# Kernel tuning notes

Hardware: AMD Instinct MI355X
Metric: run time of the kernel (lower is better)

The kernel has to match this reference:

```python
import jax, jax.numpy as jnp
import numpy as np

H = 16          # num_attention_heads
DH = 64         # attention_head_size = hidden // heads
WINDOW = 128    # window_size
GLOBAL_RATIO = 0.1
SCALE = 1.0 / np.sqrt(DH)


def _combined_mask(seq_len):
    # sliding window: |i-j| <= window_size // 2
    pos = jnp.arange(seq_len)
    dist = pos[None, :] - pos[:, None]
    window_mask = jnp.abs(dist) <= (WINDOW // 2)
    # global tokens: first max(1, int(S * ratio)) positions, full row+col
    num_global = max(1, int(seq_len * GLOBAL_RATIO))
    is_global = pos < num_global
    global_mask = is_global[:, None] | is_global[None, :]
    return window_mask | global_mask  # [S, S] bool


def setup_inputs() -> dict:
    key = jax.random.key(0)
    ks = jax.random.split(key, 9)
    B, S, Dm = 2, 2048, 1024
    s = 0.02
    return {
        "hidden_states": jax.random.normal(ks[0], (B, S, Dm), jnp.float32),
        "Wq": jax.random.normal(ks[1], (Dm, Dm), jnp.float32) * s,
        "bq": jax.random.normal(ks[2], (Dm,), jnp.float32) * s,
        "Wk": jax.random.normal(ks[3], (Dm, Dm), jnp.float32) * s,
        "bk": jax.random.normal(ks[4], (Dm,), jnp.float32) * s,
        "Wv": jax.random.normal(ks[5], (Dm, Dm), jnp.float32) * s,
        "bv": jax.random.normal(ks[6], (Dm,), jnp.float32) * s,
        "Wo": jax.random.normal(ks[7], (Dm, Dm), jnp.float32) * s,
        "bo": jax.random.normal(ks[8], (Dm,), jnp.float32) * s,
    }


def reference(hidden_states, Wq, bq, Wk, bk, Wv, bv, Wo, bo):
    B, S, Dm = hidden_states.shape

    def heads(x):  # [B,S,Dm] -> [B,H,S,Dh]
        return x.reshape(B, S, H, DH).transpose(0, 2, 1, 3)

    q = heads(hidden_states @ Wq.T + bq)
    k = heads(hidden_states @ Wk.T + bk)
    v = heads(hidden_states @ Wv.T + bv)

    scores = jnp.einsum("bhqd,bhkd->bhqk", q, k) * SCALE
    mask = _combined_mask(S)  # [S,S] bool, True = attend
    scores = scores + jnp.where(mask, 0.0, -10000.0)[None, None]

    probs = jax.nn.softmax(scores, axis=-1)
    ctx = jnp.einsum("bhqk,bhkd->bhqd", probs, v)
    ctx = ctx.transpose(0, 2, 1, 3).reshape(B, S, Dm)
    return ctx @ Wo.T + bo
```

## Files before the change

### kernel.cpp

```cpp
#include <hip/hip_runtime.h>


#define B_   2
#define S_   2048
#define DM   1024
#define H_   16
#define NG   204
#define BS_  4096
#define SCL2 0.1803368801111204f
#define NEGF -3.0e38f

typedef unsigned short u16;
typedef unsigned int   u32;
typedef __attribute__((ext_vector_type(8))) short frag8;
typedef __attribute__((ext_vector_type(4))) short frag4;
typedef __attribute__((ext_vector_type(4))) float f32x4;

#define MFMA16(A, Bf, C) __builtin_amdgcn_mfma_f32_16x16x32_bf16((A), (Bf), (C), 0, 0, 0)

__device__ __forceinline__ f32x4 mfma_16x16x16_bf16(frag4 a, frag4 b, f32x4 c) {
#if defined(__HIP_DEVICE_COMPILE__)
  return __builtin_amdgcn_mfma_f32_16x16x16bf16_1k(a, b, c, 0, 0, 0);
#else
  (void)a; (void)b;
  return c;
#endif
}

#define GLD16(g, l)                                                              \
  __builtin_amdgcn_global_load_lds((const __attribute__((address_space(1))) u32*)(g), \
                                   (__attribute__((address_space(3))) u32*)(l), 16, 0, 0)
#define EXP2(x) exp2f(x)

__device__ __forceinline__ u16 f2bf(float f) {
  union { float f; u32 u; } c; c.f = f;
  u32 u = c.u + 0x7fffu + ((c.u >> 16) & 1u);
  return (u16)(u >> 16);
}
__device__ __forceinline__ u16 f2bfc(float f) {
  union { float f; u32 u; } c; c.f = f;
  return (u16)((c.u + 0x8000u) >> 16);
}

__global__ void cvt_all(const float* __restrict__ X,  const float* __restrict__ Wq,
                        const float* __restrict__ Wk, const float* __restrict__ Wv,
                        const float* __restrict__ Wo,
                        u16* Xb, u16* Wqb, u16* Wkb, u16* Wvb, u16* Wob) {
  const int chunk = blockIdx.y;
  const float* src; u16* dst;
  if (chunk < 4)      { src = X + (size_t)chunk * 1048576; dst = Xb + (size_t)chunk * 1048576; }
  else if (chunk == 4){ src = Wq; dst = Wqb; }
  else if (chunk == 5){ src = Wk; dst = Wkb; }
  else if (chunk == 6){ src = Wv; dst = Wvb; }
  else                { src = Wo; dst = Wob; }
  int i = blockIdx.x * 256 + threadIdx.x;
  float4 v = ((const float4*)src)[i];
  u32 lo = (u32)f2bf(v.x) | ((u32)f2bf(v.y) << 16);
  u32 hi = (u32)f2bf(v.z) | ((u32)f2bf(v.w) << 16);
  ((uint2*)dst)[i] = make_uint2(lo, hi);
}

__device__ __forceinline__ void gemm_mainloop(const u16* __restrict__ A, const u16* __restrict__ Bm,
                                              int bm, int bn, u16* As, u16* Bs,
                                              f32x4 acc[4][4]) {
  const int tid = threadIdx.x;
  const int wv = tid >> 6, lane = tid & 63, l15 = lane & 15, quad = lane >> 4;
  const int wm = wv & 1, wn = wv >> 1;

  const u16* gA[4]; const u16* gB[4];
#pragma unroll
  for (int c = 0; c < 4; ++c) {
    int idx = (wv * 4 + c) * 64 + lane;
    int r = idx >> 3;
    int cb = (idx & 7) ^ (r & 7);
    gA[c] = A  + (size_t)(bm + r) * DM + cb * 8;
    gB[c] = Bm + (size_t)(bn + r) * DM + cb * 8;
  }

  int offA[4][2], offB[4][2];
#pragma unroll
  for (int i = 0; i < 4; ++i)
#pragma unroll
    for (int h = 0; h < 2; ++h) {
      int mA = wm * 64 + i * 16 + l15;
      int mB = wn * 64 + i * 16 + l15;
      int cb = (quad + h * 4) ^ (l15 & 7);
      offA[i][h] = ((mA << 3) + cb) << 4;
      offB[i][h] = ((mB << 3) + cb) << 4;
    }

  for (int k0 = 0; k0 < DM; k0 += 64) {
#pragma unroll
    for (int c = 0; c < 4; ++c) {
      GLD16(gA[c] + k0, (char*)As + (wv * 4 + c) * 1024);
      GLD16(gB[c] + k0, (char*)Bs + (wv * 4 + c) * 1024);
    }
    __syncthreads();
    frag8 af[4][2], bf[4][2];
#pragma unroll
    for (int i = 0; i < 4; ++i) {
      af[i][0] = *(const frag8*)((const char*)As + offA[i][0]);
      af[i][1] = *(const frag8*)((const char*)As + offA[i][1]);
      bf[i][0] = *(const frag8*)((const char*)Bs + offB[i][0]);
      bf[i][1] = *(const frag8*)((const char*)Bs + offB[i][1]);
    }
#pragma unroll
    for (int h = 0; h < 2; ++h)
#pragma unroll
      for (int i = 0; i < 4; ++i)
#pragma unroll
        for (int j = 0; j < 4; ++j)
          acc[i][j] = MFMA16(af[i][h], bf[j][h], acc[i][j]);
    __syncthreads();
  }
}

__global__ __launch_bounds__(256, 3) void gemm_qkv(const u16* __restrict__ Xb,
    const u16* __restrict__ Wqb, const u16* __restrict__ Wkb, const u16* __restrict__ Wvb,
    const float* __restrict__ bq, const float* __restrict__ bk, const float* __restrict__ bv,
    u16* __restrict__ Qb, u16* __restrict__ Kb, u16* __restrict__ Vt) {
  __shared__ u16 As[8192], Bs[8192];
  const int bm = blockIdx.y * 128;
  const int which = blockIdx.x >> 3;
  const int bnl = (blockIdx.x & 7) * 128;
  const u16* W = (which == 0) ? Wqb : (which == 1) ? Wkb : Wvb;
  const float* bias = (which == 0) ? bq : (which == 1) ? bk : bv;

  f32x4 acc[4][4] = {};
  gemm_mainloop(Xb, W, bm, bnl, As, Bs, acc);

  const int tid = threadIdx.x, wv = tid >> 6, lane = tid & 63, l15 = lane & 15, quad = lane >> 4;
  const int wm = wv & 1, wn = wv >> 1;
  if (which < 2) {
    u16* O = (which == 0) ? Qb : Kb;
#pragma unroll
    for (int j = 0; j < 4; ++j) {
      int col = bnl + wn * 64 + j * 16 + l15;
      float bb = bias[col];
#pragma unroll
      for (int i = 0; i < 4; ++i) {
        int row0 = bm + wm * 64 + i * 16 + quad * 4;
#pragma unroll
        for (int r = 0; r < 4; ++r)
          O[(size_t)(row0 + r) * DM + col] = f2bf(acc[i][j][r] + bb);
      }
    }
  } else {
#pragma unroll
    for (int j = 0; j < 4; ++j) {
      int col = bnl + wn * 64 + j * 16 + l15;
      float bb = bias[col];
#pragma unroll
      for (int i = 0; i < 4; ++i) {
        int row0 = bm + wm * 64 + i * 16 + quad * 4;
        u32 lo = (u32)f2bf(acc[i][j][0] + bb) | ((u32)f2bf(acc[i][j][1] + bb) << 16);
        u32 hi = (u32)f2bf(acc[i][j][2] + bb) | ((u32)f2bf(acc[i][j][3] + bb) << 16);
        *(uint2*)&Vt[(size_t)col * BS_ + row0] = make_uint2(lo, hi);
      }
    }
  }
}

__global__ __launch_bounds__(256, 3) void gemm_wo(const u16* __restrict__ Cx,
    const u16* __restrict__ Wob, const float* __restrict__ bo, float* __restrict__ out) {
  __shared__ u16 As[4096], Bs[8192];
  const int tid = threadIdx.x;
  const int wv = tid >> 6, lane = tid & 63, l15 = lane & 15, quad = lane >> 4;
  const int bm = blockIdx.y * 64, bn = blockIdx.x * 128;

  const u16* gA[2]; const u16* gB[4];
  int ldsA[2], ldsB[4];
#pragma unroll
  for (int c = 0; c < 2; ++c) {
    int slot = c * 256 + wv * 64 + lane;
    int r = slot >> 3, cb = (slot & 7) ^ (r & 7);
    gA[c] = Cx + (size_t)(bm + r) * DM + cb * 8;
    ldsA[c] = (c * 256 + wv * 64) * 16;
  }
#pragma unroll
  for (int c = 0; c < 4; ++c) {
    int slot = c * 256 + wv * 64 + lane;
    int r = slot >> 3, cb = (slot & 7) ^ (r & 7);
    gB[c] = Wob + (size_t)(bn + r) * DM + cb * 8;
    ldsB[c] = (c * 256 + wv * 64) * 16;
  }

  int offA[2], offB[8][2];
#pragma unroll
  for (int h = 0; h < 2; ++h) {
    int rowA = wv * 16 + l15;
    offA[h] = ((rowA << 3) + ((quad + h * 4) ^ (l15 & 7))) << 4;
#pragma unroll
    for (int j = 0; j < 8; ++j) {
      int rowB = j * 16 + l15;
      offB[j][h] = ((rowB << 3) + ((quad + h * 4) ^ (l15 & 7))) << 4;
    }
  }

  f32x4 acc[8] = {};
  for (int k0 = 0; k0 < DM; k0 += 64) {
#pragma unroll
    for (int c = 0; c < 2; ++c) GLD16(gA[c] + k0, (char*)As + ldsA[c]);
#pragma unroll
    for (int c = 0; c < 4; ++c) GLD16(gB[c] + k0, (char*)Bs + ldsB[c]);
    __syncthreads();
    frag8 af0 = *(const frag8*)((const char*)As + offA[0]);
    frag8 af1 = *(const frag8*)((const char*)As + offA[1]);
#pragma unroll
    for (int j = 0; j < 8; ++j) {
      frag8 bf0 = *(const frag8*)((const char*)Bs + offB[j][0]);
      frag8 bf1 = *(const frag8*)((const char*)Bs + offB[j][1]);
      acc[j] = MFMA16(af0, bf0, acc[j]);
      acc[j] = MFMA16(af1, bf1, acc[j]);
    }
    __syncthreads();
  }

#pragma unroll
  for (int j = 0; j < 8; ++j) {
    int col = bn + j * 16 + l15;
    float bb = bo[col];
    int row0 = bm + wv * 16 + quad * 4;
#pragma unroll
    for (int r = 0; r < 4; ++r)
      out[(size_t)(row0 + r) * DM + col] = acc[j][r] + bb;
  }
}

__global__ __launch_bounds__(256, 4) void attn_kernel(const u16* __restrict__ Q,
                                                      const u16* __restrict__ K,
                                                      const u16* __restrict__ Vt,
                                                      u16* __restrict__ Ctx) {
  __shared__ u16 Ks[2][4096];
  __shared__ u16 Vs[2][4096];

  const int tid = threadIdx.x, w = tid >> 6, lane = tid & 63, l15 = lane & 15, quad = lane >> 4;
  const int blk = blockIdx.x;
  const int xcd = blk & 7, slot = blk >> 3;
  const int bh = xcd + 8 * (slot & 3);
  const int strip = slot >> 2;
  const int b = bh >> 4, h = bh & 15;
  const int q0 = strip * 64;
  const int qw = q0 + w * 16;

  const u16* qrow = Q + (size_t)(b * S_ + qw + l15) * DM + h * 64;
  frag8 bq0 = *(const frag8*)(qrow + quad * 8);
  frag8 bq1 = *(const frag8*)(qrow + quad * 8 + 32);

  const u16* gK[2]; const u16* gV[2]; int ldso[2];
#pragma unroll
  for (int c = 0; c < 2; ++c) {
    int sl = (w * 2 + c) * 64 + lane;
    int r = sl >> 3, cb = (sl & 7) ^ (r & 7);
    gK[c] = K  + (size_t)(b * S_ + r) * DM + h * 64 + cb * 8;
    gV[c] = Vt + (size_t)(h * 64 + r) * BS_ + (size_t)b * S_ + cb * 8;
    ldso[c] = (w * 2 + c) * 1024;
  }

  int offKb[2];
#pragma unroll
  for (int hh = 0; hh < 2; ++hh)
    offKb[hh] = ((l15 << 3) + ((quad + hh * 4) ^ (l15 & 7))) << 4;
  int offVb[4];
#pragma unroll
  for (int kg = 0; kg < 4; ++kg)
    offVb[kg] = ((((l15 << 3) + (((kg << 1) | (quad >> 1)) ^ (l15 & 7))) << 4)
                 | ((quad & 1) << 3));

  const int qidx = qw + l15;
  const bool qglob = qidx < NG;

  f32x4 o[4] = {};
  float lsum = 0.f;

  auto activef = [&](int t) {
    int k0 = t * 64;
    return (q0 < NG) || (k0 < NG) || (k0 + 63 >= q0 - 64 && k0 <= q0 + 127);
  };
  auto nextt = [&](int cur) { int n = cur + 1; while (n < 32 && !activef(n)) ++n; return n; };
  auto stage = [&](int t, int buf) {
#pragma unroll
    for (int c = 0; c < 2; ++c) {
      GLD16(gK[c] + (size_t)t * 64 * DM, (char*)Ks[buf] + ldso[c]);
      GLD16(gV[c] + t * 64,              (char*)Vs[buf] + ldso[c]);
    }
  };

  int kt = 0, p = 0;
  stage(0, 0);
  for (;;) {
    int ktn = nextt(kt);
    bool more = ktn < 32;
    __syncthreads();
    if (more) stage(ktn, p ^ 1);

    const char* kb_ = (const char*)Ks[p];
    const char* vb_ = (const char*)Vs[p];

    f32x4 st[4] = {};
#pragma unroll
    for (int kg = 0; kg < 4; ++kg) {
      frag8 ak0 = *(const frag8*)(kb_ + offKb[0] + kg * 2048);
      frag8 ak1 = *(const frag8*)(kb_ + offKb[1] + kg * 2048);
      st[kg] = MFMA16(ak0, bq0, st[kg]);
      st[kg] = MFMA16(ak1, bq1, st[kg]);
    }

    const int k0 = kt * 64;
    const bool domask = (strip > 2) && (kt > 2);
    frag4 pk[4];
    if (domask) {
#pragma unroll
      for (int kg = 0; kg < 4; ++kg) {
        float pr[4];
#pragma unroll
        for (int r = 0; r < 4; ++r) {
          int kc = k0 + kg * 16 + quad * 4 + r;
          int d = qidx - kc;
          bool act = ((unsigned)(d + 64) <= 128u) || qglob || (kc < NG);
          float pv = EXP2(act ? st[kg][r] * SCL2 : NEGF);
          pr[r] = pv; lsum += pv;
        }
        pk[kg] = frag4{(short)f2bfc(pr[0]), (short)f2bfc(pr[1]),
                       (short)f2bfc(pr[2]), (short)f2bfc(pr[3])};
      }
    } else {
#pragma unroll
      for (int kg = 0; kg < 4; ++kg) {
        float pr[4];
#pragma unroll
        for (int r = 0; r < 4; ++r) {
          float pv = EXP2(st[kg][r] * SCL2);
          pr[r] = pv; lsum += pv;
        }
        pk[kg] = frag4{(short)f2bfc(pr[0]), (short)f2bfc(pr[1]),
                       (short)f2bfc(pr[2]), (short)f2bfc(pr[3])};
      }
    }

#pragma unroll
    for (int nt = 0; nt < 4; ++nt)
#pragma unroll
      for (int kg = 0; kg < 4; ++kg) {
        frag4 av = *(const frag4*)(vb_ + offVb[kg] + nt * 2048);
        o[nt] = mfma_16x16x16_bf16(av, pk[kg], o[nt]);
      }

    if (!more) break;
    kt = ktn; p ^= 1;
  }

  lsum += __shfl_xor(lsum, 16);
  lsum += __shfl_xor(lsum, 32);
  float inv = 1.0f / lsum;

  u16* crow = Ctx + (size_t)((size_t)b * S_ + qw + l15) * DM + h * 64;
#pragma unroll
  for (int nt = 0; nt < 4; ++nt) {
    u32 lo = (u32)f2bf(o[nt][0] * inv) | ((u32)f2bf(o[nt][1] * inv) << 16);
    u32 hi = (u32)f2bf(o[nt][2] * inv) | ((u32)f2bf(o[nt][3] * inv) << 16);
    *(uint2*)&crow[nt * 16 + quad * 4] = make_uint2(lo, hi);
  }
}

extern "C" void kernel_launch(void* const* d_in, const int* in_sizes, int n_in,
                              void* d_out, int out_size, void* d_ws, size_t ws_size,
                              hipStream_t stream) {
  const float* X  = (const float*)d_in[0];
  const float* Wq = (const float*)d_in[1];
  const float* bq = (const float*)d_in[2];
  const float* Wk = (const float*)d_in[3];
  const float* bk = (const float*)d_in[4];
  const float* Wv = (const float*)d_in[5];
  const float* bv = (const float*)d_in[6];
  const float* Wo = (const float*)d_in[7];
  const float* bo = (const float*)d_in[8];
  float* out = (float*)d_out;

  u16* ws = (u16*)d_ws;
  const size_t NX = (size_t)BS_ * DM;
  const size_t NW = (size_t)DM * DM;
  u16* Xb  = ws;
  u16* Wqb = Xb + NX;
  u16* Wkb = Wqb + NW;
  u16* Wvb = Wkb + NW;
  u16* Wob = Wvb + NW;
  u16* Qb  = Wob + NW;
  u16* Kb  = Qb + NX;
  u16* Vt  = Kb + NX;
  u16* Cx  = Vt + NX;

  cvt_all<<<dim3(1024, 8), 256, 0, stream>>>(X, Wq, Wk, Wv, Wo, Xb, Wqb, Wkb, Wvb, Wob);
  gemm_qkv<<<dim3(24, 32), 256, 0, stream>>>(Xb, Wqb, Wkb, Wvb, bq, bk, bv, Qb, Kb, Vt);
  attn_kernel<<<1024, 256, 0, stream>>>(Qb, Kb, Vt, Cx);
  gemm_wo<<<dim3(8, 64), 256, 0, stream>>>(Cx, Wob, bo, out);
}
```

Baseline: 179.9 us.

## Split heavy global-query attention strips across key segments and combine partials

The first four query strips contain global rows and must attend to all 32 key tiles. These strips are now split into four key segments, each handled by its own block, which write unnormalized partial outputs and row sums to workspace. A new combine kernel sums the partials and normalizes them. The softmax scale is folded into Q in the QKV GEMM epilogue. Row sums are computed with an MFMA against a ones vector, and the LDS swizzle and launch bounds also change. The goal is to remove the load imbalance from the long-running global strips, at the cost of an extra kernel launch and fp32 partial traffic.

```diff
diff --git a/kernel.cpp b/kernel.cpp
--- a/kernel.cpp
+++ b/kernel.cpp
@@ -133,6 +133,7 @@
   const int wm = wv & 1, wn = wv >> 1;
   if (which < 2) {
     u16* O = (which == 0) ? Qb : Kb;
+    const float scl = (which == 0) ? SCL2 : 1.0f;
 #pragma unroll
     for (int j = 0; j < 4; ++j) {
       int col = bnl + wn * 64 + j * 16 + l15;
@@ -142,7 +143,7 @@
         int row0 = bm + wm * 64 + i * 16 + quad * 4;
 #pragma unroll
         for (int r = 0; r < 4; ++r)
-          O[(size_t)(row0 + r) * DM + col] = f2bf(acc[i][j][r] + bb);
+          O[(size_t)(row0 + r) * DM + col] = f2bf((acc[i][j][r] + bb) * scl);
       }
     }
   } else {
@@ -227,19 +228,21 @@
   }
 }
 
-__global__ __launch_bounds__(256, 4) void attn_kernel(const u16* __restrict__ Q,
-                                                      const u16* __restrict__ K,
-                                                      const u16* __restrict__ Vt,
-                                                      u16* __restrict__ Ctx) {
+__global__ __launch_bounds__(256) void attn_kernel(const u16* __restrict__ Q,
+                                                   const u16* __restrict__ K,
+                                                   const u16* __restrict__ Vt,
+                                                   u16* __restrict__ Ctx,
+                                                   float* __restrict__ Op,
+                                                   float* __restrict__ Lp) {
   __shared__ u16 Ks[2][4096];
   __shared__ u16 Vs[2][4096];
 
   const int tid = threadIdx.x, w = tid >> 6, lane = tid & 63, l15 = lane & 15, quad = lane >> 4;
   const int blk = blockIdx.x;
-  const int xcd = blk & 7, slot = blk >> 3;
-  const int bh = xcd + 8 * (slot & 3);
-  const int strip = slot >> 2;
+  const int bh = blk & 31, unit = blk >> 5;
   const int b = bh >> 4, h = bh & 15;
+  const bool heavy = unit < 16;
+  const int strip = heavy ? (unit >> 2) : (unit - 12);
   const int q0 = strip * 64;
   const int qw = q0 + w * 16;
 
@@ -251,33 +254,32 @@
 #pragma unroll
   for (int c = 0; c < 2; ++c) {
     int sl = (w * 2 + c) * 64 + lane;
-    int r = sl >> 3, cb = (sl & 7) ^ (r & 7);
+    int r = sl >> 3;
+    int fr = (r & 7) ^ (((r >> 3) & 1) << 2);
+    int cb = (sl & 7) ^ fr;
     gK[c] = K  + (size_t)(b * S_ + r) * DM + h * 64 + cb * 8;
     gV[c] = Vt + (size_t)(h * 64 + r) * BS_ + (size_t)b * S_ + cb * 8;
     ldso[c] = (w * 2 + c) * 1024;
   }
 
+  const int fl = (l15 & 7) ^ (((l15 >> 3) & 1) << 2);
   int offKb[2];
 #pragma unroll
   for (int hh = 0; hh < 2; ++hh)
-    offKb[hh] = ((l15 << 3) + ((quad + hh * 4) ^ (l15 & 7))) << 4;
+    offKb[hh] = ((l15 << 3) + ((quad + hh * 4) ^ fl)) << 4;
   int offVb[4];
 #pragma unroll
   for (int kg = 0; kg < 4; ++kg)
-    offVb[kg] = ((((l15 << 3) + (((kg << 1) | (quad >> 1)) ^ (l15 & 7))) << 4)
+    offVb[kg] = ((((l15 << 3) + ((((kg << 1) | (quad >> 1))) ^ fl)) << 4)
                  | ((quad & 1) << 3));
 
   const int qidx = qw + l15;
   const bool qglob = qidx < NG;
+  const frag4 ones = {(short)0x3F80, (short)0x3F80, (short)0x3F80, (short)0x3F80};
 
   f32x4 o[4] = {};
-  float lsum = 0.f;
-
-  auto activef = [&](int t) {
-    int k0 = t * 64;
-    return (q0 < NG) || (k0 < NG) || (k0 + 63 >= q0 - 64 && k0 <= q0 + 127);
-  };
-  auto nextt = [&](int cur) { int n = cur + 1; while (n < 32 && !activef(n)) ++n; return n; };
+  f32x4 o_l = {};
+
   auto stage = [&](int t, int buf) {
 #pragma unroll
     for (int c = 0; c < 2; ++c) {
@@ -285,6 +287,83 @@
       GLD16(gV[c] + t * 64,              (char*)Vs[buf] + ldso[c]);
     }
   };
+
+  auto step = [&](int kt, int p, bool domask) {
+    const char* kb_ = (const char*)Ks[p];
+    const char* vb_ = (const char*)Vs[p];
+    f32x4 st[4] = {};
+#pragma unroll
+    for (int kg = 0; kg < 4; ++kg) {
+      frag8 ak0 = *(const frag8*)(kb_ + offKb[0] + kg * 2048);
+      frag8 ak1 = *(const frag8*)(kb_ + offKb[1] + kg * 2048);
+      st[kg] = MFMA16(ak0, bq0, st[kg]);
+      st[kg] = MFMA16(ak1, bq1, st[kg]);
+    }
+    const int k0 = kt * 64;
+    frag4 pk[4];
+    if (domask) {
+#pragma unroll
+      for (int kg = 0; kg < 4; ++kg) {
+        float pr[4];
+#pragma unroll
+        for (int r = 0; r < 4; ++r) {
+          int kc = k0 + kg * 16 + quad * 4 + r;
+          int d = qidx - kc;
+          bool act = ((unsigned)(d + 64) <= 128u) || qglob || (kc < NG);
+          pr[r] = EXP2(act ? st[kg][r] : NEGF);
+        }
+        pk[kg] = frag4{(short)f2bfc(pr[0]), (short)f2bfc(pr[1]),
+                       (short)f2bfc(pr[2]), (short)f2bfc(pr[3])};
+      }
+    } else {
+#pragma unroll
+      for (int kg = 0; kg < 4; ++kg) {
+        float pr[4];
+#pragma unroll
+        for (int r = 0; r < 4; ++r) pr[r] = EXP2(st[kg][r]);
+        pk[kg] = frag4{(short)f2bfc(pr[0]), (short)f2bfc(pr[1]),
+                       (short)f2bfc(pr[2]), (short)f2bfc(pr[3])};
+      }
+    }
+#pragma unroll
+    for (int kg = 0; kg < 4; ++kg) {
+      o_l = mfma_16x16x16_bf16(ones, pk[kg], o_l);
+#pragma unroll
+      for (int nt = 0; nt < 4; ++nt) {
+        frag4 av = *(const frag4*)(vb_ + offVb[kg] + nt * 2048);
+        o[nt] = mfma_16x16x16_bf16(av, pk[kg], o[nt]);
+      }
+    }
+  };
+
+  if (heavy) {
+    const int seg = unit & 3;
+    const int kt0 = seg * 8;
+    const bool dm = (strip == 3);
+    int p = 0;
+    stage(kt0, 0);
+#pragma unroll 1
+    for (int tt = 0; tt < 8; ++tt) {
+      __syncthreads();
+      if (tt < 7) stage(kt0 + tt + 1, p ^ 1);
+      step(kt0 + tt, p, dm && (kt0 + tt > 2));
+      p ^= 1;
+    }
+    float* op = Op + ((size_t)((bh * 4 + strip) * 4 + seg)) * 4096;
+    float* lp = Lp + ((size_t)((bh * 4 + strip) * 4 + seg)) * 64;
+    if (quad == 0) lp[w * 16 + l15] = o_l[0];
+#pragma unroll
+    for (int nt = 0; nt < 4; ++nt)
+      *(float4*)&op[(w * 16 + l15) * 64 + nt * 16 + quad * 4] =
+          make_float4(o[nt][0], o[nt][1], o[nt][2], o[nt][3]);
+    return;
+  }
+
+  auto activef = [&](int t) {
+    int k0 = t * 64;
+    return (k0 < NG) || (k0 + 63 >= q0 - 64 && k0 <= q0 + 127);
+  };
+  auto nextt = [&](int cur) { int n = cur + 1; while (n < 32 && !activef(n)) ++n; return n; };
 
   int kt = 0, p = 0;
   stage(0, 0);
@@ -293,67 +372,12 @@
     bool more = ktn < 32;
     __syncthreads();
     if (more) stage(ktn, p ^ 1);
-
-    const char* kb_ = (const char*)Ks[p];
-    const char* vb_ = (const char*)Vs[p];
-
-    f32x4 st[4] = {};
-#pragma unroll
-    for (int kg = 0; kg < 4; ++kg) {
-      frag8 ak0 = *(const frag8*)(kb_ + offKb[0] + kg * 2048);
-      frag8 ak1 = *(const frag8*)(kb_ + offKb[1] + kg * 2048);
-      st[kg] = MFMA16(ak0, bq0, st[kg]);
-      st[kg] = MFMA16(ak1, bq1, st[kg]);
-    }
-
-    const int k0 = kt * 64;
-    const bool domask = (strip > 2) && (kt > 2);
-    frag4 pk[4];
-    if (domask) {
-#pragma unroll
-      for (int kg = 0; kg < 4; ++kg) {
-        float pr[4];
-#pragma unroll
-        for (int r = 0; r < 4; ++r) {
-          int kc = k0 + kg * 16 + quad * 4 + r;
-          int d = qidx - kc;
-          bool act = ((unsigned)(d + 64) <= 128u) || qglob || (kc < NG);
-          float pv = EXP2(act ? st[kg][r] * SCL2 : NEGF);
-          pr[r] = pv; lsum += pv;
-        }
-        pk[kg] = frag4{(short)f2bfc(pr[0]), (short)f2bfc(pr[1]),
-                       (short)f2bfc(pr[2]), (short)f2bfc(pr[3])};
-      }
-    } else {
-#pragma unroll
-      for (int kg = 0; kg < 4; ++kg) {
-        float pr[4];
-#pragma unroll
-        for (int r = 0; r < 4; ++r) {
-          float pv = EXP2(st[kg][r] * SCL2);
-          pr[r] = pv; lsum += pv;
-        }
-        pk[kg] = frag4{(short)f2bfc(pr[0]), (short)f2bfc(pr[1]),
-                       (short)f2bfc(pr[2]), (short)f2bfc(pr[3])};
-      }
-    }
-
-#pragma unroll
-    for (int nt = 0; nt < 4; ++nt)
-#pragma unroll
-      for (int kg = 0; kg < 4; ++kg) {
-        frag4 av = *(const frag4*)(vb_ + offVb[kg] + nt * 2048);
-        o[nt] = mfma_16x16x16_bf16(av, pk[kg], o[nt]);
-      }
-
+    step(kt, p, kt > 2);
     if (!more) break;
     kt = ktn; p ^= 1;
   }
 
-  lsum += __shfl_xor(lsum, 16);
-  lsum += __shfl_xor(lsum, 32);
-  float inv = 1.0f / lsum;
-
+  float inv = 1.0f / o_l[0];
   u16* crow = Ctx + (size_t)((size_t)b * S_ + qw + l15) * DM + h * 64;
 #pragma unroll
   for (int nt = 0; nt < 4; ++nt) {
@@ -361,6 +385,37 @@
     u32 hi = (u32)f2bf(o[nt][2] * inv) | ((u32)f2bf(o[nt][3] * inv) << 16);
     *(uint2*)&crow[nt * 16 + quad * 4] = make_uint2(lo, hi);
   }
+}
+
+__global__ __launch_bounds__(256) void combine_kernel(const float* __restrict__ Op,
+                                                      const float* __restrict__ Lp,
+                                                      u16* __restrict__ Ctx) {
+  const int blk = blockIdx.x;
+  const int bh = blk & 31, strip = blk >> 5;
+  const int b = bh >> 4, h = bh & 15;
+  const int t = threadIdx.x;
+  const int row = t >> 2, colg = (t & 3) * 16;
+
+  const float* opb = Op + ((size_t)(bh * 4 + strip) * 4) * 4096;
+  const float* lpb = Lp + ((size_t)(bh * 4 + strip) * 4) * 64;
+
+  float l = lpb[row] + lpb[64 + row] + lpb[128 + row] + lpb[192 + row];
+  float acc[16];
+#pragma unroll
+  for (int e = 0; e < 16; ++e) acc[e] = opb[row * 64 + colg + e];
+#pragma unroll
+  for (int seg = 1; seg < 4; ++seg)
+#pragma unroll
+    for (int e = 0; e < 16; ++e) acc[e] += opb[seg * 4096 + row * 64 + colg + e];
+
+  float inv = 1.0f / l;
+  u32 pk[8];
+#pragma unroll
+  for (int p = 0; p < 8; ++p)
+    pk[p] = (u32)f2bf(acc[2 * p] * inv) | ((u32)f2bf(acc[2 * p + 1] * inv) << 16);
+  u16* dst = Ctx + (size_t)((size_t)b * S_ + strip * 64 + row) * DM + h * 64 + colg;
+  *(uint4*)dst       = make_uint4(pk[0], pk[1], pk[2], pk[3]);
+  *(uint4*)(dst + 8) = make_uint4(pk[4], pk[5], pk[6], pk[7]);
 }
 
 extern "C" void kernel_launch(void* const* d_in, const int* in_sizes, int n_in,
@@ -389,9 +444,12 @@
   u16* Kb  = Qb + NX;
   u16* Vt  = Kb + NX;
   u16* Cx  = Vt + NX;
+  float* Op = (float*)(Cx + NX);
+  float* Lp = Op + (size_t)32 * 4 * 4 * 4096;
 
   cvt_all<<<dim3(1024, 8), 256, 0, stream>>>(X, Wq, Wk, Wv, Wo, Xb, Wqb, Wkb, Wvb, Wob);
   gemm_qkv<<<dim3(24, 32), 256, 0, stream>>>(Xb, Wqb, Wkb, Wvb, bq, bk, bv, Qb, Kb, Vt);
-  attn_kernel<<<1024, 256, 0, stream>>>(Qb, Kb, Vt, Cx);
+  attn_kernel<<<44 * 32, 256, 0, stream>>>(Qb, Kb, Vt, Cx, Op, Lp);
+  combine_kernel<<<128, 256, 0, stream>>>(Op, Lp, Cx);
   gemm_wo<<<dim3(8, 64), 256, 0, stream>>>(Cx, Wob, bo, out);
 }
```

Result: faster. 169.9 us (-5.5%).
